# Kernel tuning notes

Hardware: AMD Instinct MI355X
Metric: run time of the kernel (lower is better)

## Reference

```python
import jax, jax.numpy as jnp
import numpy as np

N_NODES = 50000
N_EDGES = 800000
NFEATS = 256
HFEATS = 256
N_TARGET = 8
NEG_SLOPE = 0.2


def setup_inputs() -> dict:
    key = jax.random.key(0)
    ks = jax.random.split(key, 16)
    s = 1.0 / np.sqrt(HFEATS)
    inp = {
        'hv': jax.random.normal(ks[0], (N_NODES, NFEATS), dtype=jnp.float32),
        'src': jax.random.randint(ks[1], (N_EDGES,), 0, N_NODES, dtype=jnp.int32),
        'dst': jax.random.randint(ks[2], (N_EDGES,), 0, N_NODES, dtype=jnp.int32),
        'W_in': jax.random.normal(ks[3], (NFEATS, HFEATS), dtype=jnp.float32) * (1.0 / np.sqrt(NFEATS)),
        'b_in': jnp.zeros((HFEATS,), dtype=jnp.float32),
        'W_ro': jax.random.normal(ks[4], (3 * HFEATS, N_TARGET), dtype=jnp.float32) * (1.0 / np.sqrt(3 * HFEATS)),
        'b_ro': jnp.zeros((N_TARGET,), dtype=jnp.float32),
    }
    for i in range(1, 4):
        k = jax.random.split(ks[4 + i], 4)
        inp[f'fc{i}'] = jax.random.normal(k[0], (HFEATS, HFEATS), dtype=jnp.float32) * s
        inp[f'al{i}'] = jax.random.normal(k[1], (HFEATS,), dtype=jnp.float32) * s
        inp[f'ar{i}'] = jax.random.normal(k[2], (HFEATS,), dtype=jnp.float32) * s
        inp[f'bias{i}'] = jnp.zeros((HFEATS,), dtype=jnp.float32)
    return inp


def _gat(h, src, dst, fc, al, ar, bias):
    # DGL GATConv, 1 head: fc proj, additive attention, edge softmax over dst, sum agg.
    feat = h @ fc                                  # [N, H]
    el = feat @ al                                 # [N]
    er = feat @ ar                                 # [N]
    e = jax.nn.leaky_relu(el[src] + er[dst], NEG_SLOPE)   # [E]
    m = jax.ops.segment_max(e, dst, num_segments=N_NODES)
    ex = jnp.exp(e - m[dst])
    denom = jax.ops.segment_sum(ex, dst, num_segments=N_NODES)
    a = ex / denom[dst]                            # [E]
    out = jax.ops.segment_sum(feat[src] * a[:, None], dst, num_segments=N_NODES)
    return out + bias


def reference(hv, src, dst, W_in, b_in, W_ro, b_ro,
              fc1, al1, ar1, bias1, fc2, al2, ar2, bias2, fc3, al3, ar3, bias3):
    h0 = hv @ W_in + b_in
    h1 = _gat(jax.nn.relu(h0), src, dst, fc1, al1, ar1, bias1)
    h2 = _gat(jax.nn.relu(h1), src, dst, fc2, al2, ar2, bias2)
    h3 = _gat(jax.nn.relu(h2), src, dst, fc3, al3, ar3, bias3)
    out = jnp.concatenate([h1, h2, h3], axis=-1) @ W_ro + b_ro
    return jax.nn.sigmoid(out)
```

## Files before the change

kernel.cpp:

```cpp
#include <hip/hip_runtime.h>
#include <hip/hip_bf16.h>
#include <math.h>

#define NNODES 50000
#define NEDGES 800000
#define HF 256
#define NEG_SLOPE 0.2f
#define CHUNK 3125
#define NBUCK 196
#define NG (NBUCK * 256)

typedef short bf16x8 __attribute__((ext_vector_type(8)));
typedef float f32x4 __attribute__((ext_vector_type(4)));
typedef float f32x2 __attribute__((ext_vector_type(2)));

__device__ __forceinline__ unsigned short f2bf(float f) {
  unsigned u = __float_as_uint(f);
  unsigned r = u + 0x7FFFu + ((u >> 16) & 1u);
  return (unsigned short)(r >> 16);
}
__device__ __forceinline__ float bf2f(unsigned short u) {
  return __uint_as_float((unsigned)u << 16);
}
__device__ __forceinline__ uint2 pack4(const float* v) {
  uint2 r;
  r.x = (unsigned)f2bf(v[0]) | ((unsigned)f2bf(v[1]) << 16);
  r.y = (unsigned)f2bf(v[2]) | ((unsigned)f2bf(v[3]) << 16);
  return r;
}
__device__ __forceinline__ uint4 pack8(const float* v) {
  uint4 r;
  r.x = (unsigned)f2bf(v[0]) | ((unsigned)f2bf(v[1]) << 16);
  r.y = (unsigned)f2bf(v[2]) | ((unsigned)f2bf(v[3]) << 16);
  r.z = (unsigned)f2bf(v[4]) | ((unsigned)f2bf(v[5]) << 16);
  r.w = (unsigned)f2bf(v[6]) | ((unsigned)f2bf(v[7]) << 16);
  return r;
}

__device__ __forceinline__ int permc(int p) {
  return (p & 192) | ((p & 3) << 4) | ((p & 63) >> 2);
}

#define GLOAD_LDS16(gsrc, ldst)                                                \
  __builtin_amdgcn_global_load_lds(                                           \
      (const __attribute__((address_space(1))) unsigned int*)(const void*)(gsrc), \
      (__attribute__((address_space(3))) unsigned int*)(void*)(ldst), 16, 0, 0)

__global__ __launch_bounds__(256)
void conv_hv(const float* __restrict__ x, unsigned short* __restrict__ o) {
  size_t i = (size_t)(blockIdx.x * 256 + threadIdx.x) * 8;
  float4 a = *(const float4*)(x + i);
  float4 b = *(const float4*)(x + i + 4);
  float v[8] = {a.x, a.y, a.z, a.w, b.x, b.y, b.z, b.w};
  *(uint4*)(o + i) = pack8(v);
}

__global__ __launch_bounds__(256)
void conv_wt(const float* __restrict__ W0, const float* __restrict__ W1,
             const float* __restrict__ W2, const float* __restrict__ W3,
             unsigned short* __restrict__ WT) {
  int mat = blockIdx.y;
  const float* W = mat == 0 ? W0 : (mat == 1 ? W1 : (mat == 2 ? W2 : W3));
  int i = blockIdx.x * 256 + threadIdx.x;
  int n = i >> 8, p = i & 255;
  int k = (mat == 0) ? p : permc(p);
  WT[(size_t)mat * 65536 + i] = f2bf(W[(size_t)k * 256 + n]);
}

__global__ __launch_bounds__(256)
void conv_wro(const float* __restrict__ Wro, unsigned short* __restrict__ WroT) {
  int i = blockIdx.x * 256 + threadIdx.x;
  if (i >= 16 * 768) return;
  int n = i / 768, kk = i % 768;
  int part = kk >> 8, q = kk & 255;
  float v = (n < 8) ? Wro[(size_t)((part << 8) + permc(q)) * 8 + n] : 0.f;
  WroT[i] = f2bf(v);
}

template<bool BIAS_RELU, bool DOTS>
__global__ __launch_bounds__(512, 1)
void gemm_bf16(const unsigned short* __restrict__ A, const unsigned short* __restrict__ WT,
               const float* __restrict__ bias,
               const float* __restrict__ al, const float* __restrict__ ar,
               void* __restrict__ Cv,
               float* __restrict__ el, float* __restrict__ er, int M) {
  __shared__ unsigned short Bs[256 * 256];
  __shared__ float sEl[128][4], sEr[128][4];
  const int t = threadIdx.x;
  const int lane = t & 63;
  const int w = t >> 6;
  const int band = w >> 2;
  const int quad = w & 3;
  const int fr = lane & 15, fq = lane >> 4;
  const int brow = blockIdx.x * 128;

  for (int i = 0; i < 16; i++) {
    int s0 = (i * 8 + w) * 64;
    int s = s0 + lane;
    int g = (s & ~31) | ((s & 31) ^ ((s >> 5) & 7));
    GLOAD_LDS16(WT + (size_t)g * 8, Bs + (size_t)s0 * 8);
  }

  const unsigned short* aP[4];
#pragma unroll
  for (int i = 0; i < 4; i++) {
    int row = brow + band * 64 + i * 16 + fr;
    if (row >= M) row = M - 1;
    aP[i] = A + (size_t)row * 256 + fq * 8;
  }
  int blin[4], bxor[4];
#pragma unroll
  for (int j = 0; j < 4; j++) {
    int n = quad * 64 + j * 16 + fr;
    blin[j] = n * 512 + fq * 16;
    bxor[j] = (n & 7) << 4;
  }

  f32x4 acc[4][4];
#pragma unroll
  for (int i = 0; i < 4; i++)
#pragma unroll
    for (int j = 0; j < 4; j++) acc[i][j] = (f32x4)(0.f);

  __syncthreads();

#pragma unroll
  for (int step = 0; step < 8; step++) {
    bf16x8 af[4], bfr[4];
#pragma unroll
    for (int i = 0; i < 4; i++) af[i] = *(const bf16x8*)(aP[i] + step * 32);
#pragma unroll
    for (int j = 0; j < 4; j++)
      bfr[j] = *(const bf16x8*)((const char*)Bs + ((blin[j] | (step << 6)) ^ bxor[j]));
#pragma unroll
    for (int i = 0; i < 4; i++)
#pragma unroll
      for (int j = 0; j < 4; j++)
        acc[i][j] = __builtin_amdgcn_mfma_f32_16x16x32_bf16(af[i], bfr[j], acc[i][j], 0, 0, 0);
  }

#pragma unroll
  for (int i = 0; i < 4; i++) {
#pragma unroll
    for (int r = 0; r < 4; r++) {
      int row = brow + band * 64 + i * 16 + fq * 4 + r;
      if (row < M) {
        float v[4];
#pragma unroll
        for (int j = 0; j < 4; j++) {
          float x = acc[i][j][r];
          if (BIAS_RELU) x = fmaxf(x + bias[quad * 64 + j * 16 + fr], 0.f);
          v[j] = x;
        }
        if constexpr (DOTS) {
          int pk = __builtin_amdgcn_cvt_pk_fp8_f32(v[0], v[1], 0, false);
          pk = __builtin_amdgcn_cvt_pk_fp8_f32(v[2], v[3], pk, true);
          *(unsigned*)((unsigned char*)Cv + (size_t)row * 256 + quad * 64 + fr * 4) = (unsigned)pk;
        } else {
          *(uint2*)((unsigned short*)Cv + (size_t)row * 256 + quad * 64 + fr * 4) = pack4(v);
        }
      }
    }
  }

  if constexpr (DOTS) {
    float alv[4], arv[4];
#pragma unroll
    for (int j = 0; j < 4; j++) {
      int c = quad * 64 + j * 16 + fr;
      alv[j] = al[c];
      arv[j] = ar[c];
    }
    float pel[16], per_[16];
#pragma unroll
    for (int i = 0; i < 4; i++)
#pragma unroll
      for (int r = 0; r < 4; r++) {
        float se = 0.f, sr = 0.f;
#pragma unroll
        for (int j = 0; j < 4; j++) {
          se = fmaf(acc[i][j][r], alv[j], se);
          sr = fmaf(acc[i][j][r], arv[j], sr);
        }
        pel[i * 4 + r] = se;
        per_[i * 4 + r] = sr;
      }
#pragma unroll
    for (int off = 1; off < 16; off <<= 1)
#pragma unroll
      for (int k = 0; k < 16; k++) {
        pel[k] += __shfl_xor(pel[k], off);
        per_[k] += __shfl_xor(per_[k], off);
      }
    if (fr == 0) {
#pragma unroll
      for (int i = 0; i < 4; i++)
#pragma unroll
        for (int r = 0; r < 4; r++) {
          int rl = band * 64 + i * 16 + fq * 4 + r;
          sEl[rl][quad] = pel[i * 4 + r];
          sEr[rl][quad] = per_[i * 4 + r];
        }
    }
    __syncthreads();
    if (t < 128) {
      int row = brow + t;
      if (row < M) {
        el[row] = sEl[t][0] + sEl[t][1] + sEl[t][2] + sEl[t][3];
        er[row] = sEr[t][0] + sEr[t][1] + sEr[t][2] + sEr[t][3];
      }
    }
  }
}

__global__ __launch_bounds__(256)
void hist_coarse(const int* __restrict__ dst, int* __restrict__ gh) {
  __shared__ int lh[NBUCK];
  const int t = threadIdx.x, blk = blockIdx.x;
  if (t < NBUCK) lh[t] = 0;
  __syncthreads();
  const int base = blk * CHUNK;
  for (int i = t; i < CHUNK; i += 256)
    atomicAdd(&lh[dst[base + i] >> 8], 1);
  __syncthreads();
  if (t < NBUCK) gh[t * 256 + blk] = lh[t];
}

__global__ __launch_bounds__(256)
void bsum2(const int* __restrict__ g, int* __restrict__ bsum) {
  __shared__ int sm[256];
  int t = threadIdx.x;
  sm[t] = g[blockIdx.x * 256 + t];
  __syncthreads();
  for (int off = 128; off; off >>= 1) {
    if (t < off) sm[t] += sm[t + off];
    __syncthreads();
  }
  if (t == 0) bsum[blockIdx.x] = sm[0];
}

__global__ __launch_bounds__(256)
void sscan2(const int* __restrict__ bsum, int* __restrict__ boff) {
  __shared__ int sm[256];
  int t = threadIdx.x;
  sm[t] = (t < NBUCK) ? bsum[t] : 0;
  __syncthreads();
  for (int o = 1; o < 256; o <<= 1) {
    int v = (t >= o) ? sm[t - o] : 0;
    __syncthreads();
    sm[t] += v;
    __syncthreads();
  }
  if (t < NBUCK) boff[t] = (t == 0) ? 0 : sm[t - 1];
}

__global__ __launch_bounds__(256)
void abase2(const int* __restrict__ g, const int* __restrict__ boff,
            int* __restrict__ abase) {
  __shared__ int sm[256];
  int t = threadIdx.x;
  int i = blockIdx.x * 256 + t;
  int v = g[i];
  sm[t] = v;
  __syncthreads();
  for (int o = 1; o < 256; o <<= 1) {
    int x = (t >= o) ? sm[t - o] : 0;
    __syncthreads();
    sm[t] += x;
    __syncthreads();
  }
  abase[i] = boff[blockIdx.x] + sm[t] - v;
}

__global__ __launch_bounds__(256)
void scatter_coarse(const int* __restrict__ src, const int* __restrict__ dst,
                    const int* __restrict__ abase, uint2* __restrict__ ebuf) {
  __shared__ int off[NBUCK];
  const int t = threadIdx.x, blk = blockIdx.x;
  if (t < NBUCK) off[t] = abase[t * 256 + blk];
  __syncthreads();
  const int base = blk * CHUNK;
  for (int i = t; i < CHUNK; i += 256) {
    int e = base + i;
    int d = dst[e], s = src[e];
    int p = atomicAdd(&off[d >> 8], 1);
    ebuf[p] = make_uint2((unsigned)s, (unsigned)d);
  }
}

__global__ __launch_bounds__(256)
void fine_sort(const uint2* __restrict__ ebuf, const int* __restrict__ abase,
               int* __restrict__ rowptr, int* __restrict__ col) {
  __shared__ int hist[256], pre[256], off[256];
  const int t = threadIdx.x, b = blockIdx.x;
  const int bstart = abase[b * 256];
  const int bend = (b < NBUCK - 1) ? abase[(b + 1) * 256] : NEDGES;
  hist[t] = 0;
  __syncthreads();
  for (int e = bstart + t; e < bend; e += 256)
    atomicAdd(&hist[ebuf[e].y & 255], 1);
  __syncthreads();
  pre[t] = hist[t];
  __syncthreads();
  for (int o = 1; o < 256; o <<= 1) {
    int v = (t >= o) ? pre[t - o] : 0;
    __syncthreads();
    pre[t] += v;
    __syncthreads();
  }
  const int excl = bstart + pre[t] - hist[t];
  const int node = b * 256 + t;
  if (node < NNODES) rowptr[node] = excl;
  if (node == NNODES - 1) rowptr[NNODES] = NEDGES;
  off[t] = excl;
  __syncthreads();
  for (int e = bstart + t; e < bend; e += 256) {
    uint2 ed = ebuf[e];
    int p = atomicAdd(&off[ed.y & 255], 1);
    col[p] = (int)ed.x;
  }
}

template<bool WRITE_RELU>
__global__ __launch_bounds__(256)
void gat_csr(const int* __restrict__ rowptr, const int* __restrict__ col,
             const float* __restrict__ el, const float* __restrict__ er,
             const unsigned char* __restrict__ feat8, const float* __restrict__ bias,
             unsigned short* __restrict__ h, unsigned short* __restrict__ hrelu) {
  int d = blockIdx.x * 4 + (threadIdx.x >> 6);
  int lane = threadIdx.x & 63;
  if (d >= NNODES) return;
  const int start = rowptr[d], end = rowptr[d + 1];
  float bv[4];
#pragma unroll
  for (int m = 0; m < 4; m++)
    bv[m] = bias[((lane >> 4) << 6) | (m << 4) | (lane & 15)];
  const size_t obase = (size_t)d * HF + lane * 4;
  if (start == end) {
    *(uint2*)(h + obase) = pack4(bv);
    if (WRITE_RELU) {
      float rv[4] = {fmaxf(bv[0], 0.f), fmaxf(bv[1], 0.f), fmaxf(bv[2], 0.f), fmaxf(bv[3], 0.f)};
      *(uint2*)(hrelu + obase) = pack4(rv);
    }
    return;
  }
  const float erd = er[d];

  float sm = 0.f;
  f32x2 acl = (f32x2)(0.f), ach = (f32x2)(0.f);

  for (int c0 = start; c0 < end; c0 += 64) {
    int j = c0 + lane;
    float ex = 0.f;
    int s = 0;
    if (j < end) {
      s = col[j];
      float x = el[s] + erd;
      x = x > 0.f ? x : NEG_SLOPE * x;
      ex = __expf(x);
    }
    sm += ex;
    int n = min(64, end - c0);
    for (int q = 0; q < n; q += 8) {
      int su[8];
      float eu[8];
#pragma unroll
      for (int u = 0; u < 8; u++) {
        su[u] = __builtin_amdgcn_readlane(s, q + u);
        eu[u] = __uint_as_float(
            (unsigned)__builtin_amdgcn_readlane((int)__float_as_uint(ex), q + u));
      }
      unsigned fv[8];
#pragma unroll
      for (int u = 0; u < 8; u++)
        fv[u] = *(const unsigned*)(feat8 + (size_t)su[u] * 256 + lane * 4);
#pragma unroll
      for (int u = 0; u < 8; u++) {
        f32x2 lo = __builtin_amdgcn_cvt_pk_f32_fp8((int)fv[u], false);
        f32x2 hi = __builtin_amdgcn_cvt_pk_f32_fp8((int)fv[u], true);
        f32x2 ev = {eu[u], eu[u]};
        acl = lo * ev + acl;
        ach = hi * ev + ach;
      }
    }
  }
#pragma unroll
  for (int off = 32; off; off >>= 1) sm += __shfl_xor(sm, off);

  const float rcp = 1.f / sm;
  float ov[4];
  ov[0] = fmaf(acl.x, rcp, bv[0]);
  ov[1] = fmaf(acl.y, rcp, bv[1]);
  ov[2] = fmaf(ach.x, rcp, bv[2]);
  ov[3] = fmaf(ach.y, rcp, bv[3]);
  *(uint2*)(h + obase) = pack4(ov);
  if (WRITE_RELU) {
    float rv[4] = {fmaxf(ov[0], 0.f), fmaxf(ov[1], 0.f), fmaxf(ov[2], 0.f), fmaxf(ov[3], 0.f)};
    *(uint2*)(hrelu + obase) = pack4(rv);
  }
}

__global__ __launch_bounds__(256)
void readout(const unsigned short* __restrict__ h1, const unsigned short* __restrict__ h2,
             const unsigned short* __restrict__ h3, const unsigned short* __restrict__ WroT,
             const float* __restrict__ bro, float* __restrict__ out) {
  const int t = threadIdx.x;
  const int lane = t & 63;
  const int w = t >> 6;
  const int fr = lane & 15, fq = lane >> 4;
  const int r0 = blockIdx.x * 64 + w * 16;
  if (r0 >= NNODES) return;
  const unsigned short* hs[3] = {h1, h2, h3};

  f32x4 acc = (f32x4)(0.f);
  const int koff = fq * 8;
#pragma unroll
  for (int part = 0; part < 3; ++part) {
    const unsigned short* hp = hs[part] + (size_t)(r0 + fr) * HF + koff;
    const unsigned short* wp = WroT + fr * 768 + part * 256 + koff;
#pragma unroll
    for (int kb = 0; kb < 8; ++kb) {
      bf16x8 af = *(const bf16x8*)(hp + kb * 32);
      bf16x8 bf = *(const bf16x8*)(wp + kb * 32);
      acc = __builtin_amdgcn_mfma_f32_16x16x32_bf16(af, bf, acc, 0, 0, 0);
    }
  }
  if (fr < 8) {
    const float b = bro[fr];
#pragma unroll
    for (int r = 0; r < 4; ++r) {
      int row = r0 + fq * 4 + r;
      float v = acc[r] + b;
      out[(size_t)row * 8 + fr] = 1.f / (1.f + expf(-v));
    }
  }
}

extern "C" void kernel_launch(void* const* d_in, const int* in_sizes, int n_in,
                              void* d_out, int out_size, void* d_ws, size_t ws_size,
                              hipStream_t stream) {
  const float* hv   = (const float*)d_in[0];
  const int*   src  = (const int*)d_in[1];
  const int*   dst  = (const int*)d_in[2];
  const float* W_in = (const float*)d_in[3];
  const float* b_in = (const float*)d_in[4];
  const float* W_ro = (const float*)d_in[5];
  const float* b_ro = (const float*)d_in[6];
  const float* fc[3]   = {(const float*)d_in[7],  (const float*)d_in[11], (const float*)d_in[15]};
  const float* al[3]   = {(const float*)d_in[8],  (const float*)d_in[12], (const float*)d_in[16]};
  const float* ar[3]   = {(const float*)d_in[9],  (const float*)d_in[13], (const float*)d_in[17]};
  const float* bias[3] = {(const float*)d_in[10], (const float*)d_in[14], (const float*)d_in[18]};
  float* out = (float*)d_out;

  const size_t NH = (size_t)NNODES * HF;
  unsigned short* h1    = (unsigned short*)d_ws;
  unsigned short* h2    = h1 + NH;
  unsigned short* h3    = h2 + NH;
  unsigned char*  feat8 = (unsigned char*)(h3 + NH);
  unsigned short* hrelu = (unsigned short*)(feat8 + NH);
  unsigned short* hvbf  = hrelu + NH;
  float* el   = (float*)(hvbf + NH);
  float* er   = el + NNODES;
  int* rowptr = (int*)(er + NNODES);
  int* gh     = rowptr + NNODES + 1;
  int* abase  = gh + NG;
  int* bsum   = abase + NG;
  int* boff   = bsum + 256;
  int* col    = boff + 256;
  uint2* ebuf = (uint2*)(col + NEDGES);
  unsigned short* WT = (unsigned short*)(ebuf + NEDGES);
  unsigned short* WroT = WT + 4 * 65536;

  const int gemm_grid = (NNODES + 127) / 128;
  const int gat_grid = (NNODES + 3) / 4;
  const int ro_grid = (NNODES + 63) / 64;

  conv_hv<<<(int)(NH / 2048), 256, 0, stream>>>(hv, hvbf);
  conv_wt<<<dim3(256, 4), 256, 0, stream>>>(W_in, fc[0], fc[1], fc[2], WT);
  conv_wro<<<48, 256, 0, stream>>>(W_ro, WroT);

  hist_coarse<<<256, 256, 0, stream>>>(dst, gh);
  bsum2<<<NBUCK, 256, 0, stream>>>(gh, bsum);
  sscan2<<<1, 256, 0, stream>>>(bsum, boff);
  abase2<<<NBUCK, 256, 0, stream>>>(gh, boff, abase);
  scatter_coarse<<<256, 256, 0, stream>>>(src, dst, abase, ebuf);
  fine_sort<<<NBUCK, 256, 0, stream>>>(ebuf, abase, rowptr, col);

  gemm_bf16<true, false><<<gemm_grid, 512, 0, stream>>>(
      hvbf, WT, b_in, nullptr, nullptr, hrelu, nullptr, nullptr, NNODES);

  unsigned short* houts[3] = {h1, h2, h3};
  for (int l = 0; l < 3; ++l) {
    unsigned short* hl = houts[l];
    gemm_bf16<false, true><<<gemm_grid, 512, 0, stream>>>(
        hrelu, WT + (size_t)(l + 1) * 65536, nullptr, al[l], ar[l], feat8, el, er, NNODES);
    if (l < 2)
      gat_csr<true><<<gat_grid, 256, 0, stream>>>(rowptr, col, el, er, feat8, bias[l], hl, hrelu);
    else
      gat_csr<false><<<gat_grid, 256, 0, stream>>>(rowptr, col, el, er, feat8, bias[l], hl, hrelu);
  }

  readout<<<ro_grid, 256, 0, stream>>>(h1, h2, h3, WroT, b_ro, out);
}
```

Before: 294.9 us.

## Split GEMM over two column blocks and pack sorted edges into one word

The GEMM grid now covers two 128-column halves of the output. This halves shared memory per block (64KB to 32KB) and the accumulator count, so several blocks can fit per CU. The partial el/er attention dots from each half are combined with float atomics into buffers zeroed by a memset before each layer. Separately, the edge buffer for the sort packs the source index and the low byte of the destination into one 32-bit word, halving the scatter and fine-sort traffic. The cost is that each block re-reads the A tile for both halves, plus the extra memsets and atomics.

```diff
diff --git a/kernel.cpp b/kernel.cpp
--- a/kernel.cpp
+++ b/kernel.cpp
@@ -78,136 +78,126 @@
 }
 
 template<bool BIAS_RELU, bool DOTS>
-__global__ __launch_bounds__(512, 1)
+__global__ __launch_bounds__(512, 4)
 void gemm_bf16(const unsigned short* __restrict__ A, const unsigned short* __restrict__ WT,
                const float* __restrict__ bias,
                const float* __restrict__ al, const float* __restrict__ ar,
                void* __restrict__ Cv,
                float* __restrict__ el, float* __restrict__ er, int M) {
-  __shared__ unsigned short Bs[256 * 256];
+  __shared__ unsigned short Bs[128 * 256];
   __shared__ float sEl[128][4], sEr[128][4];
   const int t = threadIdx.x;
   const int lane = t & 63;
   const int w = t >> 6;
-  const int band = w >> 2;
-  const int quad = w & 3;
+  const int rb = w >> 2;
+  const int cs = w & 3;
   const int fr = lane & 15, fq = lane >> 4;
   const int brow = blockIdx.x * 128;
-
-  for (int i = 0; i < 16; i++) {
-    int s0 = (i * 8 + w) * 64;
+  const int cb = blockIdx.y;
+
+#pragma unroll
+  for (int i = 0; i < 8; i++) {
+    int s0 = i * 512 + w * 64;
     int s = s0 + lane;
-    int g = (s & ~31) | ((s & 31) ^ ((s >> 5) & 7));
-    GLOAD_LDS16(WT + (size_t)g * 8, Bs + (size_t)s0 * 8);
+    int gr = s >> 5;
+    int gk = (s & 31) ^ (gr & 7);
+    GLOAD_LDS16(WT + (size_t)(cb * 128 + gr) * 256 + gk * 8, Bs + (size_t)s0 * 8);
   }
 
   const unsigned short* aP[4];
 #pragma unroll
   for (int i = 0; i < 4; i++) {
-    int row = brow + band * 64 + i * 16 + fr;
+    int row = brow + rb * 64 + i * 16 + fr;
     if (row >= M) row = M - 1;
     aP[i] = A + (size_t)row * 256 + fq * 8;
   }
-  int blin[4], bxor[4];
-#pragma unroll
-  for (int j = 0; j < 4; j++) {
-    int n = quad * 64 + j * 16 + fr;
+  int blin[2], bxor[2];
+#pragma unroll
+  for (int j = 0; j < 2; j++) {
+    int n = cs * 32 + j * 16 + fr;
     blin[j] = n * 512 + fq * 16;
     bxor[j] = (n & 7) << 4;
   }
 
-  f32x4 acc[4][4];
+  f32x4 acc[4][2];
 #pragma unroll
   for (int i = 0; i < 4; i++)
 #pragma unroll
-    for (int j = 0; j < 4; j++) acc[i][j] = (f32x4)(0.f);
+    for (int j = 0; j < 2; j++) acc[i][j] = (f32x4)(0.f);
 
   __syncthreads();
 
 #pragma unroll
   for (int step = 0; step < 8; step++) {
-    bf16x8 af[4], bfr[4];
+    bf16x8 af[4], bfr[2];
 #pragma unroll
     for (int i = 0; i < 4; i++) af[i] = *(const bf16x8*)(aP[i] + step * 32);
 #pragma unroll
-    for (int j = 0; j < 4; j++)
+    for (int j = 0; j < 2; j++)
       bfr[j] = *(const bf16x8*)((const char*)Bs + ((blin[j] | (step << 6)) ^ bxor[j]));
 #pragma unroll
     for (int i = 0; i < 4; i++)
 #pragma unroll
-      for (int j = 0; j < 4; j++)
+      for (int j = 0; j < 2; j++)
         acc[i][j] = __builtin_amdgcn_mfma_f32_16x16x32_bf16(af[i], bfr[j], acc[i][j], 0, 0, 0);
   }
 
+  const int pbase = cb * 128 + ((cs >> 1) << 6) + fr * 4 + ((cs & 1) << 1);
 #pragma unroll
   for (int i = 0; i < 4; i++) {
 #pragma unroll
     for (int r = 0; r < 4; r++) {
-      int row = brow + band * 64 + i * 16 + fq * 4 + r;
+      int row = brow + rb * 64 + i * 16 + fq * 4 + r;
       if (row < M) {
-        float v[4];
-#pragma unroll
-        for (int j = 0; j < 4; j++) {
-          float x = acc[i][j][r];
-          if (BIAS_RELU) x = fmaxf(x + bias[quad * 64 + j * 16 + fr], 0.f);
-          v[j] = x;
+        float v0 = acc[i][0][r], v1 = acc[i][1][r];
+        if (BIAS_RELU) {
+          v0 = fmaxf(v0 + bias[cb * 128 + cs * 32 + 0 * 16 + fr], 0.f);
+          v1 = fmaxf(v1 + bias[cb * 128 + cs * 32 + 1 * 16 + fr], 0.f);
         }
         if constexpr (DOTS) {
-          int pk = __builtin_amdgcn_cvt_pk_fp8_f32(v[0], v[1], 0, false);
-          pk = __builtin_amdgcn_cvt_pk_fp8_f32(v[2], v[3], pk, true);
-          *(unsigned*)((unsigned char*)Cv + (size_t)row * 256 + quad * 64 + fr * 4) = (unsigned)pk;
+          int pk = __builtin_amdgcn_cvt_pk_fp8_f32(v0, v1, 0, false);
+          *(unsigned short*)((unsigned char*)Cv + (size_t)row * 256 + pbase) =
+              (unsigned short)(pk & 0xffff);
         } else {
-          *(uint2*)((unsigned short*)Cv + (size_t)row * 256 + quad * 64 + fr * 4) = pack4(v);
+          *(unsigned*)((unsigned short*)Cv + (size_t)row * 256 + pbase) =
+              (unsigned)f2bf(v0) | ((unsigned)f2bf(v1) << 16);
         }
       }
     }
   }
 
   if constexpr (DOTS) {
-    float alv[4], arv[4];
-#pragma unroll
-    for (int j = 0; j < 4; j++) {
-      int c = quad * 64 + j * 16 + fr;
+    float alv[2], arv[2];
+#pragma unroll
+    for (int j = 0; j < 2; j++) {
+      int c = cb * 128 + cs * 32 + j * 16 + fr;
       alv[j] = al[c];
       arv[j] = ar[c];
     }
-    float pel[16], per_[16];
-#pragma unroll
-    for (int i = 0; i < 4; i++)
+#pragma unroll
+    for (int i = 0; i < 4; i++) {
 #pragma unroll
       for (int r = 0; r < 4; r++) {
-        float se = 0.f, sr = 0.f;
-#pragma unroll
-        for (int j = 0; j < 4; j++) {
-          se = fmaf(acc[i][j][r], alv[j], se);
-          sr = fmaf(acc[i][j][r], arv[j], sr);
+        float se = fmaf(acc[i][0][r], alv[0], acc[i][1][r] * alv[1]);
+        float sr = fmaf(acc[i][0][r], arv[0], acc[i][1][r] * arv[1]);
+#pragma unroll
+        for (int off = 1; off < 16; off <<= 1) {
+          se += __shfl_xor(se, off);
+          sr += __shfl_xor(sr, off);
         }
-        pel[i * 4 + r] = se;
-        per_[i * 4 + r] = sr;
+        if (fr == 0) {
+          int rl = rb * 64 + i * 16 + fq * 4 + r;
+          sEl[rl][cs] = se;
+          sEr[rl][cs] = sr;
+        }
       }
-#pragma unroll
-    for (int off = 1; off < 16; off <<= 1)
-#pragma unroll
-      for (int k = 0; k < 16; k++) {
-        pel[k] += __shfl_xor(pel[k], off);
-        per_[k] += __shfl_xor(per_[k], off);
-      }
-    if (fr == 0) {
-#pragma unroll
-      for (int i = 0; i < 4; i++)
-#pragma unroll
-        for (int r = 0; r < 4; r++) {
-          int rl = band * 64 + i * 16 + fq * 4 + r;
-          sEl[rl][quad] = pel[i * 4 + r];
-          sEr[rl][quad] = per_[i * 4 + r];
-        }
     }
     __syncthreads();
     if (t < 128) {
       int row = brow + t;
       if (row < M) {
-        el[row] = sEl[t][0] + sEl[t][1] + sEl[t][2] + sEl[t][3];
-        er[row] = sEr[t][0] + sEr[t][1] + sEr[t][2] + sEr[t][3];
+        unsafeAtomicAdd(el + row, sEl[t][0] + sEl[t][1] + sEl[t][2] + sEl[t][3]);
+        unsafeAtomicAdd(er + row, sEr[t][0] + sEr[t][1] + sEr[t][2] + sEr[t][3]);
       }
     }
   }
@@ -274,7 +264,7 @@
 
 __global__ __launch_bounds__(256)
 void scatter_coarse(const int* __restrict__ src, const int* __restrict__ dst,
-                    const int* __restrict__ abase, uint2* __restrict__ ebuf) {
+                    const int* __restrict__ abase, unsigned* __restrict__ ebuf) {
   __shared__ int off[NBUCK];
   const int t = threadIdx.x, blk = blockIdx.x;
   if (t < NBUCK) off[t] = abase[t * 256 + blk];
@@ -284,12 +274,12 @@
     int e = base + i;
     int d = dst[e], s = src[e];
     int p = atomicAdd(&off[d >> 8], 1);
-    ebuf[p] = make_uint2((unsigned)s, (unsigned)d);
-  }
-}
-
-__global__ __launch_bounds__(256)
-void fine_sort(const uint2* __restrict__ ebuf, const int* __restrict__ abase,
+    ebuf[p] = ((unsigned)s << 8) | (unsigned)(d & 255);
+  }
+}
+
+__global__ __launch_bounds__(256)
+void fine_sort(const unsigned* __restrict__ ebuf, const int* __restrict__ abase,
                int* __restrict__ rowptr, int* __restrict__ col) {
   __shared__ int hist[256], pre[256], off[256];
   const int t = threadIdx.x, b = blockIdx.x;
@@ -298,7 +288,7 @@
   hist[t] = 0;
   __syncthreads();
   for (int e = bstart + t; e < bend; e += 256)
-    atomicAdd(&hist[ebuf[e].y & 255], 1);
+    atomicAdd(&hist[ebuf[e] & 255u], 1);
   __syncthreads();
   pre[t] = hist[t];
   __syncthreads();
@@ -315,9 +305,9 @@
   off[t] = excl;
   __syncthreads();
   for (int e = bstart + t; e < bend; e += 256) {
-    uint2 ed = ebuf[e];
-    int p = atomicAdd(&off[ed.y & 255], 1);
-    col[p] = (int)ed.x;
+    unsigned ed = ebuf[e];
+    int p = atomicAdd(&off[ed & 255u], 1);
+    col[p] = (int)(ed >> 8);
   }
 }
 
@@ -467,11 +457,11 @@
   int* bsum   = abase + NG;
   int* boff   = bsum + 256;
   int* col    = boff + 256;
-  uint2* ebuf = (uint2*)(col + NEDGES);
+  unsigned* ebuf = (unsigned*)(col + NEDGES);
   unsigned short* WT = (unsigned short*)(ebuf + NEDGES);
   unsigned short* WroT = WT + 4 * 65536;
 
-  const int gemm_grid = (NNODES + 127) / 128;
+  const dim3 gemm_grid((NNODES + 127) / 128, 2);
   const int gat_grid = (NNODES + 3) / 4;
   const int ro_grid = (NNODES + 63) / 64;
 
@@ -492,6 +482,7 @@
   unsigned short* houts[3] = {h1, h2, h3};
   for (int l = 0; l < 3; ++l) {
     unsigned short* hl = houts[l];
+    hipMemsetAsync(el, 0, 2 * NNODES * sizeof(float), stream);
     gemm_bf16<false, true><<<gemm_grid, 512, 0, stream>>>(
         hrelu, WT + (size_t)(l + 1) * 65536, nullptr, al[l], ar[l], feat8, el, er, NNODES);
     if (l < 2)
```

Result: slower. 353.8 us (+20.0%).
